# Kernel optimization log

Measured on AMD Instinct MI355X. Metric: run time of the kernel, lower is better.

The kernel has to match this reference:

```python
import jax, jax.numpy as jnp
import numpy as np

BN_EPS = 1e-5
NEG_SLOPE = 0.2


def _add_self_loops(edge_index, n):
    loops = jnp.arange(n, dtype=edge_index.dtype)
    src = jnp.concatenate([edge_index[0], loops])
    dst = jnp.concatenate([edge_index[1], loops])
    return src, dst


def _batchnorm(h, g, b):
    mean = h.mean(axis=0)
    var = h.var(axis=0)  # biased, as in BN forward
    return (h - mean) * jax.lax.rsqrt(var + BN_EPS) * g + b


def _gat_conv(x, edge_index, W, att_src, att_dst, bias):
    # heads=2, concat=False (mean over heads), add_self_loops=True
    n = x.shape[0]
    H, F = att_src.shape
    xp = (x @ W).reshape(n, H, F)                      # [N,H,F]
    a_src = jnp.einsum('nhf,hf->nh', xp, att_src)      # [N,H]
    a_dst = jnp.einsum('nhf,hf->nh', xp, att_dst)
    src, dst = _add_self_loops(edge_index, n)
    e = jax.nn.leaky_relu(a_src[src] + a_dst[dst], NEG_SLOPE)  # [Et,H]
    emax = jax.ops.segment_max(e, dst, num_segments=n)[dst]
    ex = jnp.exp(e - emax)
    denom = jax.ops.segment_sum(ex, dst, num_segments=n)[dst]
    alpha = ex / denom                                 # softmax per dst node
    msg = xp[src] * alpha[..., None]                   # [Et,H,F]
    out = jax.ops.segment_sum(msg, dst, num_segments=n)
    return out.mean(axis=1) + bias                     # [N,F]


def _gcn_conv(x, edge_index, W, bias):
    n = x.shape[0]
    xp = x @ W
    src, dst = _add_self_loops(edge_index, n)
    deg = jax.ops.segment_sum(jnp.ones_like(src, dtype=xp.dtype), dst, num_segments=n)
    dinv = jnp.where(deg > 0, jax.lax.rsqrt(jnp.maximum(deg, 1.0)), 0.0)
    norm = dinv[src] * dinv[dst]                       # [Et]
    out = jax.ops.segment_sum(xp[src] * norm[:, None], dst, num_segments=n)
    return out + bias


def setup_inputs() -> dict:
    key = jax.random.key(0)
    ks = jax.random.split(key, 16)
    N, E, D_IN, HID, LAT, DEC = 50000, 800000, 256, 128, 64, 256
    s = lambda fan: 1.0 / np.sqrt(fan)
    inp = {
        'x': jax.random.normal(ks[0], (N, D_IN), jnp.float32),
        'edge_index': jax.random.randint(ks[1], (2, E), 0, N, dtype=jnp.int32),
        'gat_W': jax.random.normal(ks[2], (D_IN, 2 * HID), jnp.float32) * s(D_IN),
        'gat_att_src': jax.random.normal(ks[3], (2, HID), jnp.float32) * s(HID),
        'gat_att_dst': jax.random.normal(ks[4], (2, HID), jnp.float32) * s(HID),
        'gat_bias': jnp.zeros((HID,), jnp.float32),
        'bn1_g': jnp.ones((HID,), jnp.float32),
        'bn1_b': jnp.zeros((HID,), jnp.float32),
        'gcn_W': jax.random.normal(ks[5], (HID, LAT), jnp.float32) * s(HID),
        'gcn_bias': jnp.zeros((LAT,), jnp.float32),
        'bn2_g': jnp.ones((LAT,), jnp.float32),
        'bn2_b': jnp.zeros((LAT,), jnp.float32),
        'mu_W': jax.random.normal(ks[6], (LAT, LAT), jnp.float32) * s(LAT),
        'mu_b': jnp.zeros((LAT,), jnp.float32),
        'lv_W': jax.random.normal(ks[7], (LAT, LAT), jnp.float32) * s(LAT),
        'lv_b': jnp.zeros((LAT,), jnp.float32),
        'res_W': jax.random.normal(ks[8], (LAT, LAT), jnp.float32) * s(LAT),
        'res_b': jnp.zeros((LAT,), jnp.float32),
        'dec_W1': jax.random.normal(ks[9], (2 * LAT, DEC), jnp.float32) * s(2 * LAT),
        'dec_b1': jnp.zeros((DEC,), jnp.float32),
        'dec_W2': jax.random.normal(ks[10], (DEC, 1), jnp.float32) * s(DEC),
        'dec_b2': jnp.zeros((1,), jnp.float32),
        'eps': jax.random.normal(ks[11], (N, LAT), jnp.float32),
    }
    return inp


def reference(x, edge_index, gat_W, gat_att_src, gat_att_dst, gat_bias,
              bn1_g, bn1_b, gcn_W, gcn_bias, bn2_g, bn2_b,
              mu_W, mu_b, lv_W, lv_b, res_W, res_b,
              dec_W1, dec_b1, dec_W2, dec_b2, eps):
    # encode (dropout omitted: eval mode; BN uses batch statistics)
    h = jax.nn.relu(_gat_conv(x, edge_index, gat_W, gat_att_src, gat_att_dst, gat_bias))
    h = _batchnorm(h, bn1_g, bn1_b)
    h = jax.nn.relu(_gcn_conv(h, edge_index, gcn_W, gcn_bias))
    h = _batchnorm(h, bn2_g, bn2_b)
    mu = h @ mu_W + mu_b
    logvar = h @ lv_W + lv_b
    # reparameterize
    z = mu + eps * jnp.exp(0.5 * logvar)
    # decode: edge-gather -> residual linear -> concat -> MLP
    res_z = z @ res_W + res_b
    row, col = edge_index[0], edge_index[1]
    e_emb = jnp.concatenate([res_z[row], res_z[col]], axis=1)  # [E, 2*LAT]
    hdec = jax.nn.relu(e_emb @ dec_W1 + dec_b1)
    recon = (hdec @ dec_W2 + dec_b2)[:, 0]
    return recon, mu, logvar
```

## Files before the change

### kernel.cpp

```cpp
#include <hip/hip_runtime.h>
#include <math.h>

constexpr int DIN = 256;
constexpr int HID = 128;
constexpr int LAT = 64;

typedef short bfrag __attribute__((ext_vector_type(8)));
typedef float f32x4 __attribute__((ext_vector_type(4)));

__device__ __forceinline__ float4 ld4(const float* p) { return *reinterpret_cast<const float4*>(p); }
__device__ __forceinline__ void st4(float* p, float4 v) { *reinterpret_cast<float4*>(p) = v; }

__device__ __forceinline__ unsigned short f2bf(float f) {
  unsigned int u = __float_as_uint(f);
  unsigned int r = (u + 0x7FFFu + ((u >> 16) & 1u)) >> 16;
  return (unsigned short)r;
}

__device__ __forceinline__ float bf2f(unsigned short u) {
  return __uint_as_float(((unsigned int)u) << 16);
}

__global__ __launch_bounds__(256) void gemm64(const float* __restrict__ A, const float* __restrict__ B,
                                              const float* __restrict__ crow, float* __restrict__ C,
                                              int M, int N, int K) {
  __shared__ float As[32][68];
  __shared__ float Bs[32][68];
  int t = threadIdx.x;
  int m0 = blockIdx.x * 64, n0 = blockIdx.y * 64;
  int tm = t & 15, tn = t >> 4;
  float acc[4][4];
#pragma unroll
  for (int i = 0; i < 4; i++)
#pragma unroll
    for (int j = 0; j < 4; j++) acc[i][j] = 0.f;

  for (int kt = 0; kt < K; kt += 32) {
#pragma unroll
    for (int i = 0; i < 2; ++i) {
      int f4 = t + i * 256;
      int m = f4 >> 3;
      int k4 = (f4 & 7) << 2;
      int gm = m0 + m;
      float4 v = make_float4(0.f, 0.f, 0.f, 0.f);
      if (gm < M) v = ld4(A + (size_t)gm * K + kt + k4);
      As[k4 + 0][m] = v.x; As[k4 + 1][m] = v.y; As[k4 + 2][m] = v.z; As[k4 + 3][m] = v.w;
    }
#pragma unroll
    for (int i = 0; i < 2; ++i) {
      int f4 = t + i * 256;
      int k = f4 >> 4;
      int n4 = (f4 & 15) << 2;
      float4 v = ld4(B + (size_t)(kt + k) * N + n0 + n4);
      st4(&Bs[k][n4], v);
    }
    __syncthreads();
#pragma unroll
    for (int k = 0; k < 32; ++k) {
      float4 a = ld4(&As[k][tm << 2]);
      float4 b = ld4(&Bs[k][tn << 2]);
      float av[4] = {a.x, a.y, a.z, a.w};
      float bv[4] = {b.x, b.y, b.z, b.w};
#pragma unroll
      for (int i = 0; i < 4; i++)
#pragma unroll
        for (int j = 0; j < 4; j++) acc[i][j] = fmaf(av[i], bv[j], acc[i][j]);
    }
    __syncthreads();
  }
#pragma unroll
  for (int i = 0; i < 4; ++i) {
    int gm = m0 + (tm << 2) + i;
    if (gm < M) {
      int nb = n0 + (tn << 2);
      float4 v = make_float4(acc[i][0], acc[i][1], acc[i][2], acc[i][3]);
      if (crow) { v.x += crow[nb]; v.y += crow[nb + 1]; v.z += crow[nb + 2]; v.w += crow[nb + 3]; }
      st4(C + (size_t)gm * N + nb, v);
    }
  }
}

__global__ __launch_bounds__(256) void gemm_xp_mfma(const unsigned short* __restrict__ xb,
                                                    const unsigned short* __restrict__ Wtb,
                                                    unsigned short* __restrict__ xpb, int M) {
  __shared__ unsigned short Als[64 * 256];
  __shared__ unsigned short Bls[64 * 256];
  int t = threadIdx.x;
  int wv = t >> 6, l = t & 63, lg = l >> 4, ll = l & 15;
  int cg = blockIdx.x;
  int rt = blockIdx.y;

  {
    int row = t >> 2, seg = t & 3;
    int gr = min(rt * 64 + row, M - 1);
    const uint4* src = (const uint4*)(xb + (size_t)gr * 256 + seg * 64);
    int swz = (row & 7) << 4;
#pragma unroll
    for (int c = 0; c < 8; ++c) {
      int bo = seg * 128 + c * 16;
      *(uint4*)((char*)Als + row * 512 + (bo ^ swz)) = src[c];
    }
  }
  {
    int col = t >> 2, seg = t & 3;
    const uint4* src = (const uint4*)(Wtb + (size_t)(cg * 64 + col) * 256 + seg * 64);
    int swz = (col & 7) << 4;
#pragma unroll
    for (int c = 0; c < 8; ++c) {
      int bo = seg * 128 + c * 16;
      *(uint4*)((char*)Bls + col * 512 + (bo ^ swz)) = src[c];
    }
  }
  __syncthreads();

  f32x4 acc[4];
#pragma unroll
  for (int i = 0; i < 4; ++i) acc[i] = (f32x4){0.f, 0.f, 0.f, 0.f};

#pragma unroll
  for (int kt = 0; kt < 8; ++kt) {
    int ar = wv * 16 + ll;
    bfrag af = *(const bfrag*)((char*)Als + ar * 512 + ((kt * 64 + lg * 16) ^ ((ar & 7) << 4)));
#pragma unroll
    for (int fn = 0; fn < 4; ++fn) {
      int bc = fn * 16 + ll;
      bfrag bf = *(const bfrag*)((char*)Bls + bc * 512 + ((kt * 64 + lg * 16) ^ ((bc & 7) << 4)));
      acc[fn] = __builtin_amdgcn_mfma_f32_16x16x32_bf16(af, bf, acc[fn], 0, 0, 0);
    }
  }

#pragma unroll
  for (int fn = 0; fn < 4; ++fn) {
#pragma unroll
    for (int r = 0; r < 4; ++r) {
      int row = rt * 64 + wv * 16 + lg * 4 + r;
      if (row < M) xpb[(size_t)row * 512 + cg * 64 + fn * 16 + ll] = f2bf(acc[fn][r]);
    }
  }
}

__global__ __launch_bounds__(256) void attn_scores_bf(const unsigned short* __restrict__ xpb,
                                                      const float* __restrict__ att_src,
                                                      const float* __restrict__ att_dst,
                                                      float* __restrict__ a_src, float* __restrict__ a_dst, int N) {
  int wid = threadIdx.x >> 6, lane = threadIdx.x & 63;
  int n = blockIdx.x * 4 + wid;
  if (n >= N) return;
  int h = lane >> 5;
  int f4 = (lane & 31) << 2;
  ushort4 u = *(const ushort4*)(xpb + (size_t)n * 512 + lane * 4);
  float4 as = ld4(att_src + h * 128 + f4);
  float4 ad = ld4(att_dst + h * 128 + f4);
  float vx = bf2f(u.x), vy = bf2f(u.y), vz = bf2f(u.z), vw = bf2f(u.w);
  float ps = vx * as.x + vy * as.y + vz * as.z + vw * as.w;
  float pd = vx * ad.x + vy * ad.y + vz * ad.z + vw * ad.w;
#pragma unroll
  for (int m = 16; m >= 1; m >>= 1) { ps += __shfl_xor(ps, m); pd += __shfl_xor(pd, m); }
  if ((lane & 31) == 0) { a_src[n * 2 + h] = ps; a_dst[n * 2 + h] = pd; }
}

__global__ void deg_count(const int* __restrict__ ei, int E, int Et, int* __restrict__ deg) {
  int i = blockIdx.x * blockDim.x + threadIdx.x;
  if (i >= Et) return;
  int d = (i < E) ? ei[E + i] : (i - E);
  atomicAdd(&deg[d], 1);
}

__global__ __launch_bounds__(256) void bsum_kernel(const int* __restrict__ deg, int N, int* __restrict__ bsum) {
  int t = threadIdx.x;
  int i = blockIdx.x * 256 + t;
  int v = (i < N) ? deg[i] : 0;
#pragma unroll
  for (int m = 32; m >= 1; m >>= 1) v += __shfl_xor(v, m);
  __shared__ int sh[4];
  if ((t & 63) == 0) sh[t >> 6] = v;
  __syncthreads();
  if (t == 0) bsum[blockIdx.x] = sh[0] + sh[1] + sh[2] + sh[3];
}

__global__ __launch_bounds__(256) void bscan_kernel(int* __restrict__ bsum, int B) {
  __shared__ int sh[256];
  int t = threadIdx.x;
  int v = (t < B) ? bsum[t] : 0;
  sh[t] = v;
  __syncthreads();
  for (int d = 1; d < 256; d <<= 1) {
    int x = (t >= d) ? sh[t - d] : 0;
    __syncthreads();
    sh[t] += x;
    __syncthreads();
  }
  if (t < B) bsum[t] = sh[t] - v;
}

__global__ __launch_bounds__(256) void scan_apply(const int* __restrict__ deg, const int* __restrict__ bsum, int N,
                                                  int* __restrict__ offs, int* __restrict__ cursor,
                                                  float* __restrict__ dinv) {
  int t = threadIdx.x;
  int i = blockIdx.x * 256 + t;
  int v = (i < N) ? deg[i] : 0;
  __shared__ int sh[256];
  sh[t] = v;
  __syncthreads();
  for (int d = 1; d < 256; d <<= 1) {
    int x = (t >= d) ? sh[t - d] : 0;
    __syncthreads();
    sh[t] += x;
    __syncthreads();
  }
  if (i < N) {
    int off = bsum[blockIdx.x] + sh[t] - v;
    offs[i] = off;
    cursor[i] = off;
    dinv[i] = rsqrtf((float)v);
  }
}

__global__ void csr_fill(const int* __restrict__ ei, int E, int Et, int* __restrict__ cursor, int* __restrict__ csr) {
  int i = blockIdx.x * blockDim.x + threadIdx.x;
  if (i >= Et) return;
  int s, d;
  if (i < E) { s = ei[i]; d = ei[E + i]; } else { s = i - E; d = i - E; }
  int pos = atomicAdd(&cursor[d], 1);
  csr[pos] = s;
}

__global__ __launch_bounds__(256) void gat_softmax(const int* __restrict__ offs, const int* __restrict__ deg,
                                                   const int* __restrict__ csr, const float* __restrict__ a_src,
                                                   const float* __restrict__ a_dst, float* __restrict__ alpha, int N) {
  int wid = threadIdx.x >> 6, lane = threadIdx.x & 63;
  int n = blockIdx.x * 4 + wid;
  if (n >= N) return;
  int off = offs[n], dg = deg[n];
  float ad0 = a_dst[n * 2], ad1 = a_dst[n * 2 + 1];
  float m0 = -1e30f, m1 = -1e30f;
  for (int k = lane; k < dg; k += 64) {
    int s = csr[off + k];
    float e0 = a_src[s * 2] + ad0; e0 = e0 >= 0.f ? e0 : 0.2f * e0;
    float e1 = a_src[s * 2 + 1] + ad1; e1 = e1 >= 0.f ? e1 : 0.2f * e1;
    m0 = fmaxf(m0, e0); m1 = fmaxf(m1, e1);
  }
#pragma unroll
  for (int m = 32; m >= 1; m >>= 1) { m0 = fmaxf(m0, __shfl_xor(m0, m)); m1 = fmaxf(m1, __shfl_xor(m1, m)); }
  float s0 = 0.f, s1 = 0.f;
  float2* al2 = (float2*)alpha;
  for (int k = lane; k < dg; k += 64) {
    int s = csr[off + k];
    float e0 = a_src[s * 2] + ad0; e0 = e0 >= 0.f ? e0 : 0.2f * e0;
    float e1 = a_src[s * 2 + 1] + ad1; e1 = e1 >= 0.f ? e1 : 0.2f * e1;
    float x0 = __expf(e0 - m0), x1 = __expf(e1 - m1);
    al2[off + k] = make_float2(x0, x1);
    s0 += x0; s1 += x1;
  }
#pragma unroll
  for (int m = 32; m >= 1; m >>= 1) { s0 += __shfl_xor(s0, m); s1 += __shfl_xor(s1, m); }
  float r0 = 1.f / s0, r1 = 1.f / s1;
  for (int k = lane; k < dg; k += 64) {
    float2 v = al2[off + k];
    al2[off + k] = make_float2(v.x * r0, v.y * r1);
  }
}

__global__ __launch_bounds__(256) void gat_aggregate_bf(const int* __restrict__ offs, const int* __restrict__ deg,
                                                        const int* __restrict__ csr, const float* __restrict__ alpha,
                                                        const unsigned short* __restrict__ xpb,
                                                        const float* __restrict__ bias,
                                                        float* __restrict__ h1, int N) {
  int wid = threadIdx.x >> 6, lane = threadIdx.x & 63;
  int n = blockIdx.x * 4 + wid;
  if (n >= N) return;
  int off = offs[n], dg = deg[n];
  float4 acc = make_float4(0.f, 0.f, 0.f, 0.f);
  int f4 = lane << 2;
  bool h0 = lane < 32;
  const float2* al2 = (const float2*)alpha;
  for (int k = 0; k < dg; ++k) {
    int s = csr[off + k];
    float2 al = al2[off + k];
    float a = h0 ? al.x : al.y;
    ushort4 u = ((const ushort4*)(xpb + (size_t)s * 512))[lane];
    acc.x = fmaf(bf2f(u.x), a, acc.x);
    acc.y = fmaf(bf2f(u.y), a, acc.y);
    acc.z = fmaf(bf2f(u.z), a, acc.z);
    acc.w = fmaf(bf2f(u.w), a, acc.w);
  }
  float ox = __shfl_down(acc.x, 32);
  float oy = __shfl_down(acc.y, 32);
  float oz = __shfl_down(acc.z, 32);
  float ow = __shfl_down(acc.w, 32);
  if (h0) {
    float4 b = ld4(bias + f4);
    float4 o;
    o.x = fmaxf(0.f, (acc.x + ox) * 0.5f + b.x);
    o.y = fmaxf(0.f, (acc.y + oy) * 0.5f + b.y);
    o.z = fmaxf(0.f, (acc.z + oz) * 0.5f + b.z);
    o.w = fmaxf(0.f, (acc.w + ow) * 0.5f + b.w);
    st4(h1 + (size_t)n * 128 + f4, o);
  }
}

template <int C>
__global__ __launch_bounds__(256) void bn_stats(const float* __restrict__ h, int N, float* __restrict__ P,
                                                float* __restrict__ PS) {
  constexpr int R = 256 / C;
  __shared__ float sh[256], sh2[256];
  int t = threadIdx.x;
  int c = t % C, r = t / C;
  float s = 0.f, ss = 0.f;
  for (int n = blockIdx.x * R + r; n < N; n += gridDim.x * R) {
    float v = h[(size_t)n * C + c];
    s += v; ss += v * v;
  }
  sh[t] = s; sh2[t] = ss;
  __syncthreads();
  if (r == 0) {
#pragma unroll
    for (int i = 1; i < R; ++i) { s += sh[i * C + c]; ss += sh2[i * C + c]; }
    P[blockIdx.x * C + c] = s;
    PS[blockIdx.x * C + c] = ss;
  }
}

template <int C>
__global__ void bn_reduce(const float* __restrict__ P, const float* __restrict__ PS, int G, int N,
                          const float* __restrict__ g, const float* __restrict__ b,
                          float* __restrict__ svec, float* __restrict__ tvec) {
  int c = threadIdx.x;
  if (c >= C) return;
  float s = 0.f, ss = 0.f;
  for (int i = 0; i < G; ++i) { s += P[i * C + c]; ss += PS[i * C + c]; }
  float mean = s / N;
  float var = ss / N - mean * mean;
  float sc = g[c] * rsqrtf(var + 1e-5f);
  svec[c] = sc;
  tvec[c] = b[c] - mean * sc;
}

__global__ __launch_bounds__(256) void fold_gcn(const float* __restrict__ W, const float* __restrict__ svec,
                                                const float* __restrict__ tvec, float* __restrict__ Wf,
                                                float* __restrict__ cvec) {
  int t = threadIdx.x;
  for (int i = t; i < 128 * 64; i += 256) {
    int k = i >> 6;
    Wf[i] = svec[k] * W[i];
  }
  if (t < 64) {
    float c = 0.f;
    for (int k = 0; k < 128; ++k) c += tvec[k] * W[k * 64 + t];
    cvec[t] = c;
  }
}

__global__ __launch_bounds__(256) void fold_mulv(const float* __restrict__ Wmu, const float* __restrict__ mub,
                                                 const float* __restrict__ Wlv, const float* __restrict__ lvb,
                                                 const float* __restrict__ svec, const float* __restrict__ tvec,
                                                 float* __restrict__ Wmuf, float* __restrict__ cmu,
                                                 float* __restrict__ Wlvf, float* __restrict__ clv) {
  int t = threadIdx.x;
  for (int i = t; i < 4096; i += 256) {
    int k = i >> 6;
    Wmuf[i] = svec[k] * Wmu[i];
    Wlvf[i] = svec[k] * Wlv[i];
  }
  if (t < 64) {
    float cm = mub[t], cl = lvb[t];
    for (int k = 0; k < 64; ++k) { cm += tvec[k] * Wmu[k * 64 + t]; cl += tvec[k] * Wlv[k * 64 + t]; }
    cmu[t] = cm; clv[t] = cl;
  }
}

__global__ __launch_bounds__(256) void gcn_aggregate(const int* __restrict__ offs, const int* __restrict__ deg,
                                                     const int* __restrict__ csr, const float* __restrict__ xp2,
                                                     const float* __restrict__ dinv, const float* __restrict__ bias,
                                                     float* __restrict__ g2, int N) {
  int wid = threadIdx.x >> 6, lane = threadIdx.x & 63;
  int n = blockIdx.x * 4 + wid;
  if (n >= N) return;
  int off = offs[n], dg = deg[n];
  float acc = 0.f;
  for (int k = 0; k < dg; ++k) {
    int s = csr[off + k];
    acc = fmaf(xp2[(size_t)s * 64 + lane], dinv[s], acc);
  }
  float v = acc * dinv[n] + bias[lane];
  g2[(size_t)n * 64 + lane] = fmaxf(v, 0.f);
}

__global__ void reparam(const float* __restrict__ mu, const float* __restrict__ lv,
                        const float* __restrict__ eps, float* __restrict__ z, int total) {
  int i = blockIdx.x * blockDim.x + threadIdx.x;
  if (i >= total) return;
  z[i] = fmaf(eps[i], __expf(0.5f * lv[i]), mu[i]);
}

__global__ void cvt_bf16(const float* __restrict__ in, unsigned short* __restrict__ out, int n4) {
  int i = blockIdx.x * blockDim.x + threadIdx.x;
  if (i >= n4) return;
  float4 v = ((const float4*)in)[i];
  ushort4 o;
  o.x = f2bf(v.x); o.y = f2bf(v.y); o.z = f2bf(v.z); o.w = f2bf(v.w);
  ((ushort4*)out)[i] = o;
}

__global__ void prep_gatW(const float* __restrict__ W, unsigned short* __restrict__ Wtb) {
  int i = blockIdx.x * blockDim.x + threadIdx.x;
  if (i >= 256 * 256) return;
  int col = i >> 8, k = i & 255;
  Wtb[i] = f2bf(W[k * 256 + col]);
}

__global__ void prep_W1(const float* __restrict__ W1, unsigned short* __restrict__ W1t) {
  int i = blockIdx.x * blockDim.x + threadIdx.x;
  if (i >= 4 * 256 * 40) return;
  int kt = i / 10240;
  int rem = i - kt * 10240;
  int j = rem / 40;
  int kp = rem - j * 40;
  float v = (kp < 32) ? W1[(size_t)(kt * 32 + kp) * 256 + j] : 0.f;
  W1t[i] = f2bf(v);
}

__global__ __launch_bounds__(256) void decoder_mfma(const int* __restrict__ ei, int E,
                                                    const unsigned short* __restrict__ rzb,
                                                    const unsigned short* __restrict__ W1t,
                                                    const float* __restrict__ b1, const float* __restrict__ W2,
                                                    const float* __restrict__ b2, float* __restrict__ recon) {
  __shared__ unsigned short Als[64 * 128];
  __shared__ unsigned short Bls[256 * 40];
  __shared__ float red[4][64];
  int t = threadIdx.x;
  int wv = t >> 6, l = t & 63;
  int lg = l >> 4, ll = l & 15;
  int e0 = blockIdx.x * 64;

  {
    int e = t >> 2;
    int part = (t >> 1) & 1;
    int half = t & 1;
    int eg = e0 + e;
    if (eg >= E) eg = E - 1;
    int r = (part == 0) ? ei[eg] : ei[E + eg];
    const uint4* gsrc = (const uint4*)(rzb + (size_t)r * 64 + half * 32);
    int bo0 = part * 128 + half * 64;
    int swz = (e & 7) << 4;
#pragma unroll
    for (int c = 0; c < 4; ++c) {
      uint4 v = gsrc[c];
      int bo = bo0 + c * 16;
      *(uint4*)&Als[e * 128 + ((bo ^ swz) >> 1)] = v;
    }
  }

  f32x4 acc[4][4];
#pragma unroll
  for (int a = 0; a < 4; ++a)
#pragma unroll
    for (int b = 0; b < 4; ++b) acc[a][b] = (f32x4){0.f, 0.f, 0.f, 0.f};

  for (int kt = 0; kt < 4; ++kt) {
    __syncthreads();
    {
      const uint4* gsrc = (const uint4*)(W1t + kt * 10240);
      uint4* ldst = (uint4*)Bls;
#pragma unroll
      for (int i = 0; i < 5; ++i) ldst[t + i * 256] = gsrc[t + i * 256];
    }
    __syncthreads();

    bfrag af[4];
#pragma unroll
    for (int fm = 0; fm < 4; ++fm) {
      int e = fm * 16 + ll;
      int bo = kt * 64 + lg * 16;
      af[fm] = *(const bfrag*)&Als[e * 128 + ((bo ^ ((e & 7) << 4)) >> 1)];
    }
#pragma unroll
    for (int fn = 0; fn < 4; ++fn) {
      int j = wv * 64 + fn * 16 + ll;
      bfrag bf = *(const bfrag*)&Bls[j * 40 + lg * 8];
#pragma unroll
      for (int fm = 0; fm < 4; ++fm)
        acc[fm][fn] = __builtin_amdgcn_mfma_f32_16x16x32_bf16(af[fm], bf, acc[fm][fn], 0, 0, 0);
    }
  }

  float bj[4], wj[4];
#pragma unroll
  for (int fn = 0; fn < 4; ++fn) {
    int j = wv * 64 + fn * 16 + ll;
    bj[fn] = b1[j];
    wj[fn] = W2[j];
  }
#pragma unroll
  for (int fm = 0; fm < 4; ++fm) {
    float pr[4] = {0.f, 0.f, 0.f, 0.f};
#pragma unroll
    for (int fn = 0; fn < 4; ++fn) {
#pragma unroll
      for (int r = 0; r < 4; ++r)
        pr[r] = fmaf(fmaxf(acc[fm][fn][r] + bj[fn], 0.f), wj[fn], pr[r]);
    }
#pragma unroll
    for (int m = 8; m >= 1; m >>= 1) {
#pragma unroll
      for (int r = 0; r < 4; ++r) pr[r] += __shfl_xor(pr[r], m);
    }
    if (ll == 0) {
#pragma unroll
      for (int r = 0; r < 4; ++r) red[wv][fm * 16 + lg * 4 + r] = pr[r];
    }
  }
  __syncthreads();
  if (t < 64) {
    int eg = e0 + t;
    if (eg < E) recon[eg] = red[0][t] + red[1][t] + red[2][t] + red[3][t] + b2[0];
  }
}

extern "C" void kernel_launch(void* const* d_in, const int* in_sizes, int n_in,
                              void* d_out, int out_size, void* d_ws, size_t ws_size,
                              hipStream_t stream) {
  const float* x = (const float*)d_in[0];
  const int* ei = (const int*)d_in[1];
  const float* gat_W = (const float*)d_in[2];
  const float* att_src = (const float*)d_in[3];
  const float* att_dst = (const float*)d_in[4];
  const float* gat_bias = (const float*)d_in[5];
  const float* bn1_g = (const float*)d_in[6];
  const float* bn1_b = (const float*)d_in[7];
  const float* gcn_W = (const float*)d_in[8];
  const float* gcn_bias = (const float*)d_in[9];
  const float* bn2_g = (const float*)d_in[10];
  const float* bn2_b = (const float*)d_in[11];
  const float* mu_W = (const float*)d_in[12];
  const float* mu_b = (const float*)d_in[13];
  const float* lv_W = (const float*)d_in[14];
  const float* lv_b = (const float*)d_in[15];
  const float* res_W = (const float*)d_in[16];
  const float* res_b = (const float*)d_in[17];
  const float* dec_W1 = (const float*)d_in[18];
  const float* dec_b1 = (const float*)d_in[19];
  const float* dec_W2 = (const float*)d_in[20];
  const float* dec_b2 = (const float*)d_in[21];
  const float* eps = (const float*)d_in[22];

  int N = in_sizes[0] / DIN;
  int E = in_sizes[1] / 2;
  int Et = E + N;
  int NB = (N + 255) / 256;

  float* ws = (float*)d_ws;
  size_t off = 0;
  float* xp = ws; off += (size_t)N * 256;
  unsigned short* xpb = (unsigned short*)xp;
  float* xp2 = xp;
  float* g2 = xp + (size_t)N * 64;
  float* zb = xp + (size_t)N * 128;
  float* rz = xp + (size_t)N * 192;
  unsigned short* rzb = (unsigned short*)zb;
  float* h1 = ws + off; off += (size_t)N * 128;
  unsigned short* xb = (unsigned short*)h1;
  float* a_src = ws + off; off += (size_t)2 * N;
  float* a_dst = ws + off; off += (size_t)2 * N;
  float* alpha = ws + off; off += (size_t)Et * 2;
  float* dinv = ws + off; off += N;
  float* P = ws + off; off += 128 * 128;
  float* PS = ws + off; off += 128 * 128;
  float* svec = ws + off; off += 128;
  float* tvec = ws + off; off += 128;
  float* W2f = ws + off; off += 128 * 64;
  float* c2 = ws + off; off += 64;
  float* Wmuf = ws + off; off += 64 * 64;
  float* cmu = ws + off; off += 64;
  float* Wlvf = ws + off; off += 64 * 64;
  float* clv = ws + off; off += 64;
  unsigned short* W1t = (unsigned short*)(ws + off); off += 20480;
  unsigned short* Wtb = (unsigned short*)(ws + off); off += 32768;
  int* deg = (int*)(ws + off); off += N;
  int* offs = (int*)(ws + off); off += N;
  int* cursor = (int*)(ws + off); off += N;
  int* bsum = (int*)(ws + off); off += 256;
  int* csr = (int*)(ws + off); off += Et;

  float* recon = (float*)d_out;
  float* mu = recon + E;
  float* lv = mu + (size_t)N * LAT;

  prep_W1<<<(4 * 256 * 40 + 255) / 256, 256, 0, stream>>>(dec_W1, W1t);
  prep_gatW<<<(256 * 256 + 255) / 256, 256, 0, stream>>>(gat_W, Wtb);

  cvt_bf16<<<(N * 64 + 255) / 256, 256, 0, stream>>>(x, xb, N * 64);
  dim3 gX(4, (N + 63) / 64);
  gemm_xp_mfma<<<gX, 256, 0, stream>>>(xb, Wtb, xpb, N);

  attn_scores_bf<<<(N + 3) / 4, 256, 0, stream>>>(xpb, att_src, att_dst, a_src, a_dst, N);

  hipMemsetAsync(deg, 0, (size_t)N * sizeof(int), stream);
  deg_count<<<(Et + 255) / 256, 256, 0, stream>>>(ei, E, Et, deg);
  bsum_kernel<<<NB, 256, 0, stream>>>(deg, N, bsum);
  bscan_kernel<<<1, 256, 0, stream>>>(bsum, NB);
  scan_apply<<<NB, 256, 0, stream>>>(deg, bsum, N, offs, cursor, dinv);
  csr_fill<<<(Et + 255) / 256, 256, 0, stream>>>(ei, E, Et, cursor, csr);

  gat_softmax<<<(N + 3) / 4, 256, 0, stream>>>(offs, deg, csr, a_src, a_dst, alpha, N);
  gat_aggregate_bf<<<(N + 3) / 4, 256, 0, stream>>>(offs, deg, csr, alpha, xpb, gat_bias, h1, N);

  bn_stats<128><<<128, 256, 0, stream>>>(h1, N, P, PS);
  bn_reduce<128><<<1, 128, 0, stream>>>(P, PS, 128, N, bn1_g, bn1_b, svec, tvec);
  fold_gcn<<<1, 256, 0, stream>>>(gcn_W, svec, tvec, W2f, c2);
  dim3 gB((N + 63) / 64, 1);
  gemm64<<<gB, 256, 0, stream>>>(h1, W2f, c2, xp2, N, 64, 128);

  gcn_aggregate<<<(N + 3) / 4, 256, 0, stream>>>(offs, deg, csr, xp2, dinv, gcn_bias, g2, N);

  bn_stats<64><<<128, 256, 0, stream>>>(g2, N, P, PS);
  bn_reduce<64><<<1, 64, 0, stream>>>(P, PS, 128, N, bn2_g, bn2_b, svec, tvec);
  fold_mulv<<<1, 256, 0, stream>>>(mu_W, mu_b, lv_W, lv_b, svec, tvec, Wmuf, cmu, Wlvf, clv);
  gemm64<<<gB, 256, 0, stream>>>(g2, Wmuf, cmu, mu, N, 64, 64);
  gemm64<<<gB, 256, 0, stream>>>(g2, Wlvf, clv, lv, N, 64, 64);

  reparam<<<(N * 64 + 255) / 256, 256, 0, stream>>>(mu, lv, eps, zb, N * 64);
  gemm64<<<gB, 256, 0, stream>>>(zb, res_W, res_b, rz, N, 64, 64);
  cvt_bf16<<<(N * 16 + 255) / 256, 256, 0, stream>>>(rz, rzb, N * 16);

  decoder_mfma<<<(E + 63) / 64, 256, 0, stream>>>(ei, E, rzb, W1t, dec_b1, dec_W2, dec_b2, recon);
}
```

Baseline: 684.1 us.

## Fuse GAT softmax into aggregation and emit bf16 from small GEMMs

Merges the GAT softmax and aggregation kernels. The exponentials are recomputed inside the aggregation loop and normalised once at the end, so the per-edge alpha array is never written or read back. Adds a gemm variant that writes bf16 directly. It is used for the GCN projection, which halves the gather bytes in gcn aggregation, and for the residual projection, which removes a separate convert kernel. The costs are redundant exp work, since every lane computes the exps for each edge, and bf16 rounding of the GCN features.

```diff
diff --git a/kernel.cpp b/kernel.cpp
--- a/kernel.cpp
+++ b/kernel.cpp
@@ -76,6 +76,68 @@
       float4 v = make_float4(acc[i][0], acc[i][1], acc[i][2], acc[i][3]);
       if (crow) { v.x += crow[nb]; v.y += crow[nb + 1]; v.z += crow[nb + 2]; v.w += crow[nb + 3]; }
       st4(C + (size_t)gm * N + nb, v);
+    }
+  }
+}
+
+__global__ __launch_bounds__(256) void gemm64b(const float* __restrict__ A, const float* __restrict__ B,
+                                               const float* __restrict__ crow, unsigned short* __restrict__ Cb,
+                                               int M, int N, int K) {
+  __shared__ float As[32][68];
+  __shared__ float Bs[32][68];
+  int t = threadIdx.x;
+  int m0 = blockIdx.x * 64, n0 = blockIdx.y * 64;
+  int tm = t & 15, tn = t >> 4;
+  float acc[4][4];
+#pragma unroll
+  for (int i = 0; i < 4; i++)
+#pragma unroll
+    for (int j = 0; j < 4; j++) acc[i][j] = 0.f;
+
+  for (int kt = 0; kt < K; kt += 32) {
+#pragma unroll
+    for (int i = 0; i < 2; ++i) {
+      int f4 = t + i * 256;
+      int m = f4 >> 3;
+      int k4 = (f4 & 7) << 2;
+      int gm = m0 + m;
+      float4 v = make_float4(0.f, 0.f, 0.f, 0.f);
+      if (gm < M) v = ld4(A + (size_t)gm * K + kt + k4);
+      As[k4 + 0][m] = v.x; As[k4 + 1][m] = v.y; As[k4 + 2][m] = v.z; As[k4 + 3][m] = v.w;
+    }
+#pragma unroll
+    for (int i = 0; i < 2; ++i) {
+      int f4 = t + i * 256;
+      int k = f4 >> 4;
+      int n4 = (f4 & 15) << 2;
+      float4 v = ld4(B + (size_t)(kt + k) * N + n0 + n4);
+      st4(&Bs[k][n4], v);
+    }
+    __syncthreads();
+#pragma unroll
+    for (int k = 0; k < 32; ++k) {
+      float4 a = ld4(&As[k][tm << 2]);
+      float4 b = ld4(&Bs[k][tn << 2]);
+      float av[4] = {a.x, a.y, a.z, a.w};
+      float bv[4] = {b.x, b.y, b.z, b.w};
+#pragma unroll
+      for (int i = 0; i < 4; i++)
+#pragma unroll
+        for (int j = 0; j < 4; j++) acc[i][j] = fmaf(av[i], bv[j], acc[i][j]);
+    }
+    __syncthreads();
+  }
+#pragma unroll
+  for (int i = 0; i < 4; ++i) {
+    int gm = m0 + (tm << 2) + i;
+    if (gm < M) {
+      int nb = n0 + (tn << 2);
+      ushort4 o;
+      o.x = f2bf(acc[i][0] + crow[nb]);
+      o.y = f2bf(acc[i][1] + crow[nb + 1]);
+      o.z = f2bf(acc[i][2] + crow[nb + 2]);
+      o.w = f2bf(acc[i][3] + crow[nb + 3]);
+      *(ushort4*)(Cb + (size_t)gm * N + nb) = o;
     }
   }
 }
@@ -225,70 +287,56 @@
   csr[pos] = s;
 }
 
-__global__ __launch_bounds__(256) void gat_softmax(const int* __restrict__ offs, const int* __restrict__ deg,
-                                                   const int* __restrict__ csr, const float* __restrict__ a_src,
-                                                   const float* __restrict__ a_dst, float* __restrict__ alpha, int N) {
+__global__ __launch_bounds__(256) void gat_fused(const int* __restrict__ offs, const int* __restrict__ deg,
+                                                 const int* __restrict__ csr, const float* __restrict__ a_src,
+                                                 const float* __restrict__ a_dst,
+                                                 const unsigned short* __restrict__ xpb,
+                                                 const float* __restrict__ bias,
+                                                 float* __restrict__ h1, int N) {
   int wid = threadIdx.x >> 6, lane = threadIdx.x & 63;
   int n = blockIdx.x * 4 + wid;
   if (n >= N) return;
   int off = offs[n], dg = deg[n];
   float ad0 = a_dst[n * 2], ad1 = a_dst[n * 2 + 1];
+  const float2* as2 = (const float2*)a_src;
+
   float m0 = -1e30f, m1 = -1e30f;
   for (int k = lane; k < dg; k += 64) {
     int s = csr[off + k];
-    float e0 = a_src[s * 2] + ad0; e0 = e0 >= 0.f ? e0 : 0.2f * e0;
-    float e1 = a_src[s * 2 + 1] + ad1; e1 = e1 >= 0.f ? e1 : 0.2f * e1;
+    float2 a = as2[s];
+    float e0 = a.x + ad0; e0 = e0 >= 0.f ? e0 : 0.2f * e0;
+    float e1 = a.y + ad1; e1 = e1 >= 0.f ? e1 : 0.2f * e1;
     m0 = fmaxf(m0, e0); m1 = fmaxf(m1, e1);
   }
 #pragma unroll
   for (int m = 32; m >= 1; m >>= 1) { m0 = fmaxf(m0, __shfl_xor(m0, m)); m1 = fmaxf(m1, __shfl_xor(m1, m)); }
+
+  float4 acc = make_float4(0.f, 0.f, 0.f, 0.f);
   float s0 = 0.f, s1 = 0.f;
-  float2* al2 = (float2*)alpha;
-  for (int k = lane; k < dg; k += 64) {
-    int s = csr[off + k];
-    float e0 = a_src[s * 2] + ad0; e0 = e0 >= 0.f ? e0 : 0.2f * e0;
-    float e1 = a_src[s * 2 + 1] + ad1; e1 = e1 >= 0.f ? e1 : 0.2f * e1;
-    float x0 = __expf(e0 - m0), x1 = __expf(e1 - m1);
-    al2[off + k] = make_float2(x0, x1);
-    s0 += x0; s1 += x1;
-  }
-#pragma unroll
-  for (int m = 32; m >= 1; m >>= 1) { s0 += __shfl_xor(s0, m); s1 += __shfl_xor(s1, m); }
-  float r0 = 1.f / s0, r1 = 1.f / s1;
-  for (int k = lane; k < dg; k += 64) {
-    float2 v = al2[off + k];
-    al2[off + k] = make_float2(v.x * r0, v.y * r1);
-  }
-}
-
-__global__ __launch_bounds__(256) void gat_aggregate_bf(const int* __restrict__ offs, const int* __restrict__ deg,
-                                                        const int* __restrict__ csr, const float* __restrict__ alpha,
-                                                        const unsigned short* __restrict__ xpb,
-                                                        const float* __restrict__ bias,
-                                                        float* __restrict__ h1, int N) {
-  int wid = threadIdx.x >> 6, lane = threadIdx.x & 63;
-  int n = blockIdx.x * 4 + wid;
-  if (n >= N) return;
-  int off = offs[n], dg = deg[n];
-  float4 acc = make_float4(0.f, 0.f, 0.f, 0.f);
-  int f4 = lane << 2;
   bool h0 = lane < 32;
-  const float2* al2 = (const float2*)alpha;
   for (int k = 0; k < dg; ++k) {
     int s = csr[off + k];
-    float2 al = al2[off + k];
-    float a = h0 ? al.x : al.y;
+    float2 a = as2[s];
+    float e0 = a.x + ad0; e0 = e0 >= 0.f ? e0 : 0.2f * e0;
+    float e1 = a.y + ad1; e1 = e1 >= 0.f ? e1 : 0.2f * e1;
+    float x0 = __expf(e0 - m0), x1 = __expf(e1 - m1);
+    s0 += x0; s1 += x1;
+    float xa = h0 ? x0 : x1;
     ushort4 u = ((const ushort4*)(xpb + (size_t)s * 512))[lane];
-    acc.x = fmaf(bf2f(u.x), a, acc.x);
-    acc.y = fmaf(bf2f(u.y), a, acc.y);
-    acc.z = fmaf(bf2f(u.z), a, acc.z);
-    acc.w = fmaf(bf2f(u.w), a, acc.w);
-  }
+    acc.x = fmaf(bf2f(u.x), xa, acc.x);
+    acc.y = fmaf(bf2f(u.y), xa, acc.y);
+    acc.z = fmaf(bf2f(u.z), xa, acc.z);
+    acc.w = fmaf(bf2f(u.w), xa, acc.w);
+  }
+  float r = h0 ? (1.f / s0) : (1.f / s1);
+  acc.x *= r; acc.y *= r; acc.z *= r; acc.w *= r;
+
   float ox = __shfl_down(acc.x, 32);
   float oy = __shfl_down(acc.y, 32);
   float oz = __shfl_down(acc.z, 32);
   float ow = __shfl_down(acc.w, 32);
   if (h0) {
+    int f4 = lane << 2;
     float4 b = ld4(bias + f4);
     float4 o;
     o.x = fmaxf(0.f, (acc.x + ox) * 0.5f + b.x);
@@ -369,10 +417,11 @@
   }
 }
 
-__global__ __launch_bounds__(256) void gcn_aggregate(const int* __restrict__ offs, const int* __restrict__ deg,
-                                                     const int* __restrict__ csr, const float* __restrict__ xp2,
-                                                     const float* __restrict__ dinv, const float* __restrict__ bias,
-                                                     float* __restrict__ g2, int N) {
+__global__ __launch_bounds__(256) void gcn_aggregate_bf(const int* __restrict__ offs, const int* __restrict__ deg,
+                                                        const int* __restrict__ csr,
+                                                        const unsigned short* __restrict__ xpb2,
+                                                        const float* __restrict__ dinv, const float* __restrict__ bias,
+                                                        float* __restrict__ g2, int N) {
   int wid = threadIdx.x >> 6, lane = threadIdx.x & 63;
   int n = blockIdx.x * 4 + wid;
   if (n >= N) return;
@@ -380,7 +429,7 @@
   float acc = 0.f;
   for (int k = 0; k < dg; ++k) {
     int s = csr[off + k];
-    acc = fmaf(xp2[(size_t)s * 64 + lane], dinv[s], acc);
+    acc = fmaf(bf2f(xpb2[(size_t)s * 64 + lane]), dinv[s], acc);
   }
   float v = acc * dinv[n] + bias[lane];
   g2[(size_t)n * 64 + lane] = fmaxf(v, 0.f);
@@ -553,16 +602,15 @@
   size_t off = 0;
   float* xp = ws; off += (size_t)N * 256;
   unsigned short* xpb = (unsigned short*)xp;
-  float* xp2 = xp;
+  unsigned short* xpb2 = (unsigned short*)xp;
   float* g2 = xp + (size_t)N * 64;
   float* zb = xp + (size_t)N * 128;
   float* rz = xp + (size_t)N * 192;
-  unsigned short* rzb = (unsigned short*)zb;
+  unsigned short* rzb = (unsigned short*)rz;
   float* h1 = ws + off; off += (size_t)N * 128;
   unsigned short* xb = (unsigned short*)h1;
   float* a_src = ws + off; off += (size_t)2 * N;
   float* a_dst = ws + off; off += (size_t)2 * N;
-  float* alpha = ws + off; off += (size_t)Et * 2;
   float* dinv = ws + off; off += N;
   float* P = ws + off; off += 128 * 128;
   float* PS = ws + off; off += 128 * 128;
@@ -602,16 +650,15 @@
   scan_apply<<<NB, 256, 0, stream>>>(deg, bsum, N, offs, cursor, dinv);
   csr_fill<<<(Et + 255) / 256, 256, 0, stream>>>(ei, E, Et, cursor, csr);
 
-  gat_softmax<<<(N + 3) / 4, 256, 0, stream>>>(offs, deg, csr, a_src, a_dst, alpha, N);
-  gat_aggregate_bf<<<(N + 3) / 4, 256, 0, stream>>>(offs, deg, csr, alpha, xpb, gat_bias, h1, N);
+  gat_fused<<<(N + 3) / 4, 256, 0, stream>>>(offs, deg, csr, a_src, a_dst, xpb, gat_bias, h1, N);
 
   bn_stats<128><<<128, 256, 0, stream>>>(h1, N, P, PS);
   bn_reduce<128><<<1, 128, 0, stream>>>(P, PS, 128, N, bn1_g, bn1_b, svec, tvec);
   fold_gcn<<<1, 256, 0, stream>>>(gcn_W, svec, tvec, W2f, c2);
   dim3 gB((N + 63) / 64, 1);
-  gemm64<<<gB, 256, 0, stream>>>(h1, W2f, c2, xp2, N, 64, 128);
-
-  gcn_aggregate<<<(N + 3) / 4, 256, 0, stream>>>(offs, deg, csr, xp2, dinv, gcn_bias, g2, N);
+  gemm64b<<<gB, 256, 0, stream>>>(h1, W2f, c2, xpb2, N, 64, 128);
+
+  gcn_aggregate_bf<<<(N + 3) / 4, 256, 0, stream>>>(offs, deg, csr, xpb2, dinv, gcn_bias, g2, N);
 
   bn_stats<64><<<128, 256, 0, stream>>>(g2, N, P, PS);
   bn_reduce<64><<<1, 64, 0, stream>>>(P, PS, 128, N, bn2_g, bn2_b, svec, tvec);
@@ -620,8 +667,7 @@
   gemm64<<<gB, 256, 0, stream>>>(g2, Wlvf, clv, lv, N, 64, 64);
 
   reparam<<<(N * 64 + 255) / 256, 256, 0, stream>>>(mu, lv, eps, zb, N * 64);
-  gemm64<<<gB, 256, 0, stream>>>(zb, res_W, res_b, rz, N, 64, 64);
-  cvt_bf16<<<(N * 16 + 255) / 256, 256, 0, stream>>>(rz, rzb, N * 16);
+  gemm64b<<<gB, 256, 0, stream>>>(zb, res_W, res_b, rzb, N, 64, 64);
 
   decoder_mfma<<<(E + 63) / 64, 256, 0, stream>>>(ei, E, rzb, W1t, dec_b1, dec_W2, dec_b2, recon);
 }
```

Result: faster. 669.5 us (-2.1%).
